# Kernel optimization log

Hardware: AMD Instinct MI355X
Metric: run time of the kernel (lower is better)

Reference implementation:

```python
import jax, jax.numpy as jnp
import numpy as np

NUM_HEADS = 12


def setup_inputs() -> dict:
    key = jax.random.key(0)
    k1, k2, k3, k4 = jax.random.split(key, 4)
    dim = 768
    B, N1, N2 = 8, 64, 4096  # N1 must equal head_dim = dim // num_heads
    x = jax.random.normal(k1, (B, N1, dim), dtype=jnp.float32)
    y = jax.random.normal(k2, (B, N2, dim), dtype=jnp.float32)
    # torch nn.Linear layout: [out_features, in_features]
    W_qkv = jax.random.normal(k3, (3 * dim, dim), dtype=jnp.float32) * 0.02
    W_proj = jax.random.normal(k4, (dim, dim), dtype=jnp.float32) * 0.02
    b_proj = jnp.zeros((dim,), dtype=jnp.float32)
    return {"x": x, "y": y, "W_qkv": W_qkv, "W_proj": W_proj, "b_proj": b_proj}


def _split_heads(t, H):
    # [B, N, C] -> [B, H, N, C//H]
    B, N, C = t.shape
    return t.reshape(B, N, H, C // H).transpose(0, 2, 1, 3)


def reference(x, y, W_qkv, W_proj, b_proj):
    H = NUM_HEADS
    B1, N1, C = x.shape
    B2, N2, _ = y.shape
    hd = C // H
    scale = hd ** -0.5

    # qkv projections (bias=False); take q from x, k/v from y
    qkv_x = x @ W_qkv.T                      # [B, N1, 3C]
    q = _split_heads(qkv_x[..., :C], H)      # [B, H, N1, hd]
    qkv_y = y @ W_qkv.T                      # [B, N2, 3C]
    k = _split_heads(qkv_y[..., C:2 * C], H)  # [B, H, N2, hd]
    v = _split_heads(qkv_y[..., 2 * C:], H)   # [B, H, N2, hd]

    attn = jnp.einsum('bhqd,bhkd->bhqk', q, k) * scale  # [B, H, N1, N2]
    attn = jax.nn.softmax(attn, axis=-1)
    attn_t = attn.transpose(0, 1, 3, 2)       # [B, H, N2, N1]; N1 == hd

    # non-standard elementwise combine with v (requires N1 == hd)
    out = attn_t * v                          # [B, H, N2, hd]
    out = out.transpose(0, 2, 1, 3).reshape(B2, N2, C)
    return out @ W_proj.T + b_proj
```

## Files before the change

### kernel.cpp

```cpp
#include <hip/hip_runtime.h>
#include <math.h>


typedef __attribute__((ext_vector_type(8))) short short8;
typedef __attribute__((ext_vector_type(4))) float f32x4;

__device__ __forceinline__ ushort f2bf(float x) {
  unsigned u = __float_as_uint(x);
  u += 0x7fffu + ((u >> 16) & 1u);
  return (ushort)(u >> 16);
}
__device__ __forceinline__ float bf2f(ushort h) {
  return __uint_as_float((unsigned)h << 16);
}

__device__ __forceinline__ void gl_lds16(const ushort* g, ushort* l) {
  __builtin_amdgcn_global_load_lds(
      (__attribute__((address_space(1))) void*)g,
      (__attribute__((address_space(3))) void*)l, 16, 0, 0);
}

__global__ __launch_bounds__(256) void cast_all(
    const float* __restrict__ x, ushort* __restrict__ xb,
    const float* __restrict__ w1, ushort* __restrict__ w1b,
    const float* __restrict__ w2, ushort* __restrict__ w2b,
    const float* __restrict__ y, ushort* __restrict__ yb) {
  long i = (long)(blockIdx.x * 256 + threadIdx.x) * 8;
  if (i >= 27918336L) return;
  const float* s; ushort* d; long off;
  if (i < 393216L)        { s = x;  d = xb;  off = i; }
  else if (i < 2162688L)  { s = w1; d = w1b; off = i - 393216L; }
  else if (i < 2752512L)  { s = w2; d = w2b; off = i - 2162688L; }
  else                    { s = y;  d = yb;  off = i - 2752512L; }
  float4 a = *(const float4*)(s + off);
  float4 b = *(const float4*)(s + off + 4);
  ushort o[8] = {f2bf(a.x), f2bf(a.y), f2bf(a.z), f2bf(a.w),
                 f2bf(b.x), f2bf(b.y), f2bf(b.z), f2bf(b.w)};
  *(uint4*)(d + off) = *(const uint4*)o;
}

template <typename CT>
__device__ __forceinline__ void gemm_body(
    const ushort* __restrict__ A, int lda,
    const ushort* __restrict__ B, int ldb,
    CT* __restrict__ C, int ldc, int K,
    const float* __restrict__ bias, int rt, int ct)
{
  __shared__ __align__(16) ushort As[3][4096];
  __shared__ __align__(16) ushort Bs[3][4096];
  const int tid = threadIdx.x;
  const int m0 = rt * 128, n0 = ct * 128;

  const int w = tid >> 6, lane = tid & 63;
  const int lm = lane & 15, quad = lane >> 4;
  const int wm = (w & 1) * 64, wn = (w >> 1) * 64;

  const int G0 = w * 64 + lane, G1 = G0 + 256;
  const int r0 = G0 >> 2, c0 = ((G0 & 3) - (r0 >> 1)) & 3;
  const int r1 = G1 >> 2, c1 = ((G1 & 3) - (r1 >> 1)) & 3;
  const ushort* Ag0 = A + (size_t)(m0 + r0) * lda + c0 * 8;
  const ushort* Ag1 = A + (size_t)(m0 + r1) * lda + c1 * 8;
  const ushort* Bg0 = B + (size_t)(n0 + r0) * ldb + c0 * 8;
  const ushort* Bg1 = B + (size_t)(n0 + r1) * ldb + c1 * 8;
  const int lds0 = w * 512, lds1 = w * 512 + 2048;

  f32x4 acc[4][4];
#pragma unroll
  for (int i = 0; i < 4; ++i)
#pragma unroll
    for (int j = 0; j < 4; ++j) acc[i][j] = (f32x4)(0.f);

  const int nk = K >> 5;
  gl_lds16(Ag0, &As[0][lds0]); gl_lds16(Ag1, &As[0][lds1]);
  gl_lds16(Bg0, &Bs[0][lds0]); gl_lds16(Bg1, &Bs[0][lds1]);
  gl_lds16(Ag0 + 32, &As[1][lds0]); gl_lds16(Ag1 + 32, &As[1][lds1]);
  gl_lds16(Bg0 + 32, &Bs[1][lds0]); gl_lds16(Bg1 + 32, &Bs[1][lds1]);
  asm volatile("s_waitcnt vmcnt(4)" ::: "memory");

  for (int kk = 0; kk < nk; ++kk) {
    __builtin_amdgcn_s_barrier();
    __builtin_amdgcn_sched_barrier(0);
    if (kk + 2 < nk) {
      const int k0 = (kk + 2) << 5;
      ushort* Ad = &As[(kk + 2) % 3][0];
      ushort* Bd = &Bs[(kk + 2) % 3][0];
      gl_lds16(Ag0 + k0, Ad + lds0); gl_lds16(Ag1 + k0, Ad + lds1);
      gl_lds16(Bg0 + k0, Bd + lds0); gl_lds16(Bg1 + k0, Bd + lds1);
    }
    const ushort* Ab = &As[kk % 3][0];
    const ushort* Bb = &Bs[kk % 3][0];
    short8 af[4], bf8[4];
#pragma unroll
    for (int i = 0; i < 4; ++i) {
      const int Ra = wm + i * 16 + lm;
      af[i] = *(const short8*)(const void*)(Ab + Ra * 32 + ((quad + (Ra >> 1)) & 3) * 8);
      const int Rb = wn + i * 16 + lm;
      bf8[i] = *(const short8*)(const void*)(Bb + Rb * 32 + ((quad + (Rb >> 1)) & 3) * 8);
    }
#pragma unroll
    for (int i = 0; i < 4; ++i)
#pragma unroll
      for (int j = 0; j < 4; ++j)
        acc[i][j] = __builtin_amdgcn_mfma_f32_16x16x32_bf16(af[i], bf8[j], acc[i][j], 0, 0, 0);
    if (kk < nk - 2)       asm volatile("s_waitcnt vmcnt(4)" ::: "memory");
    else if (kk == nk - 2) asm volatile("s_waitcnt vmcnt(0)" ::: "memory");
  }
  __syncthreads();

  if constexpr (sizeof(CT) == 2) {
    ushort* eb = ((ushort*)&Bs[0][0]) + w * 2048;
#pragma unroll
    for (int i = 0; i < 4; ++i) {
      ushort* ebc = eb + (i & 1) * 1024;
#pragma unroll
      for (int j = 0; j < 4; ++j)
#pragma unroll
        for (int r = 0; r < 4; ++r) {
          const int R = quad * 4 + r;
          const int gt = j * 2 + (lm >> 3);
          const int gs = (gt + R) & 7;
          ebc[R * 64 + gs * 8 + (lm & 7)] = f2bf(acc[i][j][r]);
        }
#pragma unroll
      for (int p = 0; p < 2; ++p) {
        const int R2 = (lane >> 3) + p * 8;
        const int g = lane & 7;
        const int gt2 = (g - R2) & 7;
        uint4 v = *(const uint4*)(const void*)(ebc + R2 * 64 + g * 8);
        *(uint4*)(C + (size_t)(m0 + wm + i * 16 + R2) * ldc + n0 + wn + gt2 * 8) = v;
      }
    }
  } else {
#pragma unroll
    for (int j = 0; j < 4; ++j) {
      const int col = n0 + wn + j * 16 + lm;
      const float bb = bias ? bias[col] : 0.f;
#pragma unroll
      for (int i = 0; i < 4; ++i) {
        const int row = m0 + wm + i * 16 + quad * 4;
#pragma unroll
        for (int r = 0; r < 4; ++r)
          C[(size_t)(row + r) * ldc + col] = (CT)(acc[i][j][r] + bb);
      }
    }
  }
}

__global__ __launch_bounds__(256) void qkv_gemm(
    const ushort* __restrict__ xbf, const ushort* __restrict__ ybf,
    const ushort* __restrict__ wqkv, ushort* __restrict__ qbf,
    ushort* __restrict__ kvbf)
{
  const int id = blockIdx.x;
  const ushort *A, *B; ushort* C; int ldc, rt, ct;
  if (id < 3072) {
    const int xcd = id & 7, local = id >> 3;
    const int per = 12 * 16;
    const int grp = local / per, s = local % per;
    rt = xcd * 32 + grp * 16 + (s & 15);
    ct = s >> 4;
    A = ybf; B = wqkv + (size_t)768 * 768; C = kvbf; ldc = 1536;
  } else {
    const int id2 = id - 3072;
    rt = id2 & 3; ct = id2 >> 2;
    A = xbf; B = wqkv; C = qbf; ldc = 768;
  }
  gemm_body<ushort>(A, 768, B, 768, C, ldc, 768, nullptr, rt, ct);
}

__global__ __launch_bounds__(256) void out_gemm(
    const ushort* __restrict__ Ebf, const ushort* __restrict__ wpbf,
    const float* __restrict__ bias, float* __restrict__ out)
{
  const int id = blockIdx.x;
  const int xcd = id & 7, local = id >> 3;
  const int per = 6 * 16;
  const int grp = local / per, s = local % per;
  const int rt = xcd * 32 + grp * 16 + (s & 15);
  const int ct = s >> 4;
  gemm_body<float>(Ebf, 768, wpbf, 768, out, 768, 768, bias, rt, ct);
}

__global__ __launch_bounds__(256) void attn_pass1(
    const ushort* __restrict__ Q,
    const ushort* __restrict__ KV,
    float* __restrict__ parts)
{
  const int chunk = blockIdx.x, h = blockIdx.y, b = blockIdx.z;
  const int tid = threadIdx.x;
  __shared__ __align__(16) ushort Qs[64 * 72];
  __shared__ __align__(16) ushort Ks[128 * 72];
  __shared__ float sm[4][64], ss[4][64];
#pragma unroll
  for (int p = 0; p < 2; ++p) {
    const int G = tid + 256 * p, row = G >> 3, g = G & 7;
    *(uint4*)(Qs + row * 72 + g * 8) =
        *(const uint4*)(Q + (size_t)(b * 64 + row) * 768 + h * 64 + g * 8);
  }
#pragma unroll
  for (int p = 0; p < 4; ++p) {
    const int G = tid + 256 * p, row = G >> 3, g = G & 7;
    *(uint4*)(Ks + row * 72 + g * 8) =
        *(const uint4*)(KV + (size_t)(b * 4096 + chunk * 128 + row) * 1536 + h * 64 + g * 8);
  }
  __syncthreads();

  const int w = tid >> 6, lane = tid & 63;
  const int lm = lane & 15, quad = lane >> 4;
  const int wn = w * 32;

  f32x4 acc[4][2];
#pragma unroll
  for (int i = 0; i < 4; ++i) { acc[i][0] = (f32x4)(0.f); acc[i][1] = (f32x4)(0.f); }
#pragma unroll
  for (int s = 0; s < 2; ++s) {
    short8 qf[4], kf[2];
#pragma unroll
    for (int i = 0; i < 4; ++i)
      qf[i] = *(const short8*)(const void*)(Qs + (i * 16 + lm) * 72 + s * 32 + quad * 8);
#pragma unroll
    for (int jn = 0; jn < 2; ++jn)
      kf[jn] = *(const short8*)(const void*)(Ks + (wn + jn * 16 + lm) * 72 + s * 32 + quad * 8);
#pragma unroll
    for (int i = 0; i < 4; ++i)
#pragma unroll
      for (int jn = 0; jn < 2; ++jn)
        acc[i][jn] = __builtin_amdgcn_mfma_f32_16x16x32_bf16(qf[i], kf[jn], acc[i][jn], 0, 0, 0);
  }

#pragma unroll
  for (int i = 0; i < 4; ++i)
#pragma unroll
    for (int r = 0; r < 4; ++r) {
      float v0 = acc[i][0][r] * 0.125f, v1 = acc[i][1][r] * 0.125f;
      float m = fmaxf(v0, v1);
      m = fmaxf(m, __shfl_xor(m, 1)); m = fmaxf(m, __shfl_xor(m, 2));
      m = fmaxf(m, __shfl_xor(m, 4)); m = fmaxf(m, __shfl_xor(m, 8));
      float e = __expf(v0 - m) + __expf(v1 - m);
      e += __shfl_xor(e, 1); e += __shfl_xor(e, 2);
      e += __shfl_xor(e, 4); e += __shfl_xor(e, 8);
      if (lm == 0) {
        const int j = i * 16 + quad * 4 + r;
        sm[w][j] = m; ss[w][j] = e;
      }
    }
  __syncthreads();
  if (tid < 64) {
    float g = fmaxf(fmaxf(sm[0][tid], sm[1][tid]), fmaxf(sm[2][tid], sm[3][tid]));
    float s = ss[0][tid] * __expf(sm[0][tid] - g) + ss[1][tid] * __expf(sm[1][tid] - g)
            + ss[2][tid] * __expf(sm[2][tid] - g) + ss[3][tid] * __expf(sm[3][tid] - g);
    const int bh = b * 12 + h;
    float* p = parts + ((size_t)(bh * 32 + chunk) * 64 + tid) * 2;
    p[0] = g; p[1] = s;
  }
}

__global__ __launch_bounds__(256) void attn_pass2(
    const ushort* __restrict__ Q, const ushort* __restrict__ KV,
    const float* __restrict__ parts, ushort* __restrict__ E)
{
  const int chunk = blockIdx.x, h = blockIdx.y, b = blockIdx.z;
  const int tid = threadIdx.x;
  __shared__ __align__(16) ushort Qs[64 * 72];
  __shared__ __align__(16) ushort Ks[128 * 72];
  __shared__ __align__(16) ushort Vs[128 * 72];
  __shared__ float st[64][2];
#pragma unroll
  for (int p = 0; p < 2; ++p) {
    const int G = tid + 256 * p, row = G >> 3, g = G & 7;
    *(uint4*)(Qs + row * 72 + g * 8) =
        *(const uint4*)(Q + (size_t)(b * 64 + row) * 768 + h * 64 + g * 8);
  }
#pragma unroll
  for (int p = 0; p < 4; ++p) {
    const int G = tid + 256 * p, row = G >> 3, g = G & 7;
    const size_t rbase = (size_t)(b * 4096 + chunk * 128 + row) * 1536 + h * 64 + g * 8;
    *(uint4*)(Ks + row * 72 + g * 8) = *(const uint4*)(KV + rbase);
    *(uint4*)(Vs + row * 72 + g * 8) = *(const uint4*)(KV + rbase + 768);
  }
  {
    const int bh = b * 12 + h;
    const int tq = tid >> 2, tc = tid & 3;
    float pm[8], ps[8];
    float gm = -1e30f;
#pragma unroll
    for (int c = 0; c < 8; ++c) {
      const float* p = parts + ((size_t)(bh * 32 + tc * 8 + c) * 64 + tq) * 2;
      pm[c] = p[0]; ps[c] = p[1];
      gm = fmaxf(gm, pm[c]);
    }
    gm = fmaxf(gm, __shfl_xor(gm, 1));
    gm = fmaxf(gm, __shfl_xor(gm, 2));
    float s = 0.f;
#pragma unroll
    for (int c = 0; c < 8; ++c) s += ps[c] * __expf(pm[c] - gm);
    s += __shfl_xor(s, 1);
    s += __shfl_xor(s, 2);
    if (tc == 0) { st[tq][0] = gm; st[tq][1] = 1.f / s; }
  }
  __syncthreads();

  const int w = tid >> 6, lane = tid & 63;
  const int lm = lane & 15, quad = lane >> 4;
  const int wn = w * 32;

  f32x4 acc[4][2];
#pragma unroll
  for (int i = 0; i < 4; ++i) { acc[i][0] = (f32x4)(0.f); acc[i][1] = (f32x4)(0.f); }
#pragma unroll
  for (int s = 0; s < 2; ++s) {
    short8 qf[4], kf[2];
#pragma unroll
    for (int i = 0; i < 4; ++i)
      qf[i] = *(const short8*)(const void*)(Qs + (i * 16 + lm) * 72 + s * 32 + quad * 8);
#pragma unroll
    for (int jn = 0; jn < 2; ++jn)
      kf[jn] = *(const short8*)(const void*)(Ks + (wn + jn * 16 + lm) * 72 + s * 32 + quad * 8);
#pragma unroll
    for (int i = 0; i < 4; ++i)
#pragma unroll
      for (int jn = 0; jn < 2; ++jn)
        acc[i][jn] = __builtin_amdgcn_mfma_f32_16x16x32_bf16(qf[i], kf[jn], acc[i][jn], 0, 0, 0);
  }

  ushort ev[4][2][4];
#pragma unroll
  for (int i = 0; i < 4; ++i)
#pragma unroll
    for (int jn = 0; jn < 2; ++jn)
#pragma unroll
      for (int r = 0; r < 4; ++r) {
        const float v = acc[i][jn][r] * 0.125f;
        const int j = i * 16 + quad * 4 + r;
        const float p = __expf(v - st[j][0]) * st[j][1];
        const int key = wn + jn * 16 + lm;
        ev[i][jn][r] = f2bf(p * bf2f(Vs[key * 72 + j]));
      }
  __syncthreads();
  ushort* Es = Ks;
#pragma unroll
  for (int i = 0; i < 4; ++i)
#pragma unroll
    for (int jn = 0; jn < 2; ++jn)
#pragma unroll
      for (int r = 0; r < 4; ++r)
        Es[(wn + jn * 16 + lm) * 72 + i * 16 + quad * 4 + r] = ev[i][jn][r];
  __syncthreads();
#pragma unroll
  for (int k = 0; k < 4; ++k) {
    const int row = tid >> 1, g = (tid & 1) * 4 + k;
    uint4 v = *(const uint4*)(const void*)(Es + row * 72 + g * 8);
    *(uint4*)(E + (size_t)(b * 4096 + chunk * 128 + row) * 768 + h * 64 + g * 8) = v;
  }
}

extern "C" void kernel_launch(void* const* d_in, const int* in_sizes, int n_in,
                              void* d_out, int out_size, void* d_ws, size_t ws_size,
                              hipStream_t stream) {
  const float* x     = (const float*)d_in[0];
  const float* y     = (const float*)d_in[1];
  const float* Wqkv  = (const float*)d_in[2];
  const float* Wproj = (const float*)d_in[3];
  const float* bproj = (const float*)d_in[4];
  float* out = (float*)d_out;

  char* wsb = (char*)d_ws;
  ushort* xbf    = (ushort*)(wsb + 0);
  ushort* qbf    = (ushort*)(wsb + 786432);
  ushort* wqkvbf = (ushort*)(wsb + 1572864);
  float*  parts  = (float*)(wsb + 1572864);
  ushort* wpbf   = (ushort*)(wsb + 5111808);
  ushort* ybf    = (ushort*)(wsb + 6291456);
  ushort* Ebf    = ybf;
  ushort* KVbf   = (ushort*)(wsb + 56623104);

  cast_all<<<13632, 256, 0, stream>>>(x, xbf, Wqkv, wqkvbf, Wproj, wpbf, y, ybf);

  qkv_gemm<<<3096, 256, 0, stream>>>(xbf, ybf, wqkvbf, qbf, KVbf);

  attn_pass1<<<dim3(32, 12, 8), 256, 0, stream>>>(qbf, KVbf, parts);
  attn_pass2<<<dim3(32, 12, 8), 256, 0, stream>>>(qbf, KVbf, parts, Ebf);

  out_gemm<<<1536, 256, 0, stream>>>(Ebf, wpbf, bproj, out);
}
```

Measured before the change: 405.4 us.

## Enlarge GEMM tiles to 256x128 with double buffering and remap grids

The shared GEMM body moves from 128x128 tiles with a three-stage LDS ring to 256x128 tiles with two-stage buffering. Each wave now computes a 128x64 sub-tile of 8x4 MFMA fragments, which raises B-operand reuse and halves the number of blocks for the QKV and output projections. The explicit vmcnt waits are replaced by plain __syncthreads, and launch bounds request two blocks per CU. The risks are a shallower prefetch pipeline, higher register use from the doubled accumulators, and fewer blocks to spread across the CUs.

```diff
diff --git a/kernel.cpp b/kernel.cpp
--- a/kernel.cpp
+++ b/kernel.cpp
@@ -46,71 +46,78 @@
     CT* __restrict__ C, int ldc, int K,
     const float* __restrict__ bias, int rt, int ct)
 {
-  __shared__ __align__(16) ushort As[3][4096];
-  __shared__ __align__(16) ushort Bs[3][4096];
+  __shared__ __align__(16) ushort As[2][8192];
+  __shared__ __align__(16) ushort Bs[2][4096];
   const int tid = threadIdx.x;
-  const int m0 = rt * 128, n0 = ct * 128;
+  const int m0 = rt * 256, n0 = ct * 128;
 
   const int w = tid >> 6, lane = tid & 63;
   const int lm = lane & 15, quad = lane >> 4;
-  const int wm = (w & 1) * 64, wn = (w >> 1) * 64;
-
-  const int G0 = w * 64 + lane, G1 = G0 + 256;
-  const int r0 = G0 >> 2, c0 = ((G0 & 3) - (r0 >> 1)) & 3;
-  const int r1 = G1 >> 2, c1 = ((G1 & 3) - (r1 >> 1)) & 3;
-  const ushort* Ag0 = A + (size_t)(m0 + r0) * lda + c0 * 8;
-  const ushort* Ag1 = A + (size_t)(m0 + r1) * lda + c1 * 8;
-  const ushort* Bg0 = B + (size_t)(n0 + r0) * ldb + c0 * 8;
-  const ushort* Bg1 = B + (size_t)(n0 + r1) * ldb + c1 * 8;
-  const int lds0 = w * 512, lds1 = w * 512 + 2048;
-
-  f32x4 acc[4][4];
-#pragma unroll
-  for (int i = 0; i < 4; ++i)
+  const int WR = (w >> 1) * 128, WC = (w & 1) * 64;
+
+  const ushort* Ag[4];
+#pragma unroll
+  for (int q = 0; q < 4; ++q) {
+    const int G = q * 256 + w * 64 + lane;
+    const int row = G >> 2, g = ((G & 3) - (row >> 1)) & 3;
+    Ag[q] = A + (size_t)(m0 + row) * lda + g * 8;
+  }
+  const ushort* Bg[2];
+#pragma unroll
+  for (int q = 0; q < 2; ++q) {
+    const int G = q * 256 + w * 64 + lane;
+    const int row = G >> 2, g = ((G & 3) - (row >> 1)) & 3;
+    Bg[q] = B + (size_t)(n0 + row) * ldb + g * 8;
+  }
+
+  f32x4 acc[8][4];
+#pragma unroll
+  for (int i = 0; i < 8; ++i)
 #pragma unroll
     for (int j = 0; j < 4; ++j) acc[i][j] = (f32x4)(0.f);
 
   const int nk = K >> 5;
-  gl_lds16(Ag0, &As[0][lds0]); gl_lds16(Ag1, &As[0][lds1]);
-  gl_lds16(Bg0, &Bs[0][lds0]); gl_lds16(Bg1, &Bs[0][lds1]);
-  gl_lds16(Ag0 + 32, &As[1][lds0]); gl_lds16(Ag1 + 32, &As[1][lds1]);
-  gl_lds16(Bg0 + 32, &Bs[1][lds0]); gl_lds16(Bg1 + 32, &Bs[1][lds1]);
-  asm volatile("s_waitcnt vmcnt(4)" ::: "memory");
-
+#pragma unroll
+  for (int q = 0; q < 4; ++q) gl_lds16(Ag[q], &As[0][q * 2048 + w * 512]);
+#pragma unroll
+  for (int q = 0; q < 2; ++q) gl_lds16(Bg[q], &Bs[0][q * 2048 + w * 512]);
+
+  int cur = 0;
   for (int kk = 0; kk < nk; ++kk) {
-    __builtin_amdgcn_s_barrier();
-    __builtin_amdgcn_sched_barrier(0);
-    if (kk + 2 < nk) {
-      const int k0 = (kk + 2) << 5;
-      ushort* Ad = &As[(kk + 2) % 3][0];
-      ushort* Bd = &Bs[(kk + 2) % 3][0];
-      gl_lds16(Ag0 + k0, Ad + lds0); gl_lds16(Ag1 + k0, Ad + lds1);
-      gl_lds16(Bg0 + k0, Bd + lds0); gl_lds16(Bg1 + k0, Bd + lds1);
-    }
-    const ushort* Ab = &As[kk % 3][0];
-    const ushort* Bb = &Bs[kk % 3][0];
-    short8 af[4], bf8[4];
-#pragma unroll
-    for (int i = 0; i < 4; ++i) {
-      const int Ra = wm + i * 16 + lm;
+    __syncthreads();
+    if (kk + 1 < nk) {
+      const int k0 = (kk + 1) << 5;
+#pragma unroll
+      for (int q = 0; q < 4; ++q) gl_lds16(Ag[q] + k0, &As[cur ^ 1][q * 2048 + w * 512]);
+#pragma unroll
+      for (int q = 0; q < 2; ++q) gl_lds16(Bg[q] + k0, &Bs[cur ^ 1][q * 2048 + w * 512]);
+    }
+    const ushort* Ab = &As[cur][0];
+    const ushort* Bb = &Bs[cur][0];
+    short8 af[8], bf8[4];
+#pragma unroll
+    for (int i = 0; i < 8; ++i) {
+      const int Ra = WR + i * 16 + lm;
       af[i] = *(const short8*)(const void*)(Ab + Ra * 32 + ((quad + (Ra >> 1)) & 3) * 8);
-      const int Rb = wn + i * 16 + lm;
-      bf8[i] = *(const short8*)(const void*)(Bb + Rb * 32 + ((quad + (Rb >> 1)) & 3) * 8);
-    }
-#pragma unroll
-    for (int i = 0; i < 4; ++i)
+    }
+#pragma unroll
+    for (int j = 0; j < 4; ++j) {
+      const int Rb = WC + j * 16 + lm;
+      bf8[j] = *(const short8*)(const void*)(Bb + Rb * 32 + ((quad + (Rb >> 1)) & 3) * 8);
+    }
+#pragma unroll
+    for (int i = 0; i < 8; ++i)
 #pragma unroll
       for (int j = 0; j < 4; ++j)
         acc[i][j] = __builtin_amdgcn_mfma_f32_16x16x32_bf16(af[i], bf8[j], acc[i][j], 0, 0, 0);
-    if (kk < nk - 2)       asm volatile("s_waitcnt vmcnt(4)" ::: "memory");
-    else if (kk == nk - 2) asm volatile("s_waitcnt vmcnt(0)" ::: "memory");
+    cur ^= 1;
   }
   __syncthreads();
 
   if constexpr (sizeof(CT) == 2) {
-    ushort* eb = ((ushort*)&Bs[0][0]) + w * 2048;
-#pragma unroll
-    for (int i = 0; i < 4; ++i) {
+    ushort* eb = ((ushort*)&As[0][0]) + w * 2048;
+#pragma unroll
+    for (int i = 0; i < 8; ++i) {
       ushort* ebc = eb + (i & 1) * 1024;
 #pragma unroll
       for (int j = 0; j < 4; ++j)
@@ -127,17 +134,17 @@
         const int g = lane & 7;
         const int gt2 = (g - R2) & 7;
         uint4 v = *(const uint4*)(const void*)(ebc + R2 * 64 + g * 8);
-        *(uint4*)(C + (size_t)(m0 + wm + i * 16 + R2) * ldc + n0 + wn + gt2 * 8) = v;
+        *(uint4*)(C + (size_t)(m0 + WR + i * 16 + R2) * ldc + n0 + WC + gt2 * 8) = v;
       }
     }
   } else {
 #pragma unroll
     for (int j = 0; j < 4; ++j) {
-      const int col = n0 + wn + j * 16 + lm;
+      const int col = n0 + WC + j * 16 + lm;
       const float bb = bias ? bias[col] : 0.f;
 #pragma unroll
-      for (int i = 0; i < 4; ++i) {
-        const int row = m0 + wm + i * 16 + quad * 4;
+      for (int i = 0; i < 8; ++i) {
+        const int row = m0 + WR + i * 16 + quad * 4;
 #pragma unroll
         for (int r = 0; r < 4; ++r)
           C[(size_t)(row + r) * ldc + col] = (CT)(acc[i][j][r] + bb);
@@ -146,38 +153,32 @@
   }
 }
 
-__global__ __launch_bounds__(256) void qkv_gemm(
+__global__ __launch_bounds__(256, 2) void qkv_gemm(
     const ushort* __restrict__ xbf, const ushort* __restrict__ ybf,
     const ushort* __restrict__ wqkv, ushort* __restrict__ qbf,
     ushort* __restrict__ kvbf)
 {
   const int id = blockIdx.x;
-  const ushort *A, *B; ushort* C; int ldc, rt, ct;
-  if (id < 3072) {
+  if (id < 1536) {
     const int xcd = id & 7, local = id >> 3;
-    const int per = 12 * 16;
-    const int grp = local / per, s = local % per;
-    rt = xcd * 32 + grp * 16 + (s & 15);
-    ct = s >> 4;
-    A = ybf; B = wqkv + (size_t)768 * 768; C = kvbf; ldc = 1536;
+    const int rt = xcd * 16 + (local & 15);
+    const int ct = local >> 4;
+    gemm_body<ushort>(ybf, 768, wqkv + (size_t)768 * 768, 768, kvbf, 1536, 768,
+                      nullptr, rt, ct);
   } else {
-    const int id2 = id - 3072;
-    rt = id2 & 3; ct = id2 >> 2;
-    A = xbf; B = wqkv; C = qbf; ldc = 768;
-  }
-  gemm_body<ushort>(A, 768, B, 768, C, ldc, 768, nullptr, rt, ct);
-}
-
-__global__ __launch_bounds__(256) void out_gemm(
+    const int q = id - 1536;
+    gemm_body<ushort>(xbf, 768, wqkv, 768, qbf, 768, 768, nullptr, q & 1, q >> 1);
+  }
+}
+
+__global__ __launch_bounds__(256, 2) void out_gemm(
     const ushort* __restrict__ Ebf, const ushort* __restrict__ wpbf,
     const float* __restrict__ bias, float* __restrict__ out)
 {
   const int id = blockIdx.x;
   const int xcd = id & 7, local = id >> 3;
-  const int per = 6 * 16;
-  const int grp = local / per, s = local % per;
-  const int rt = xcd * 32 + grp * 16 + (s & 15);
-  const int ct = s >> 4;
+  const int rt = xcd * 16 + (local & 15);
+  const int ct = local >> 4;
   gemm_body<float>(Ebf, 768, wpbf, 768, out, 768, 768, bias, rt, ct);
 }
 
@@ -376,10 +377,10 @@
 
   cast_all<<<13632, 256, 0, stream>>>(x, xbf, Wqkv, wqkvbf, Wproj, wpbf, y, ybf);
 
-  qkv_gemm<<<3096, 256, 0, stream>>>(xbf, ybf, wqkvbf, qbf, KVbf);
+  qkv_gemm<<<1548, 256, 0, stream>>>(xbf, ybf, wqkvbf, qbf, KVbf);
 
   attn_pass1<<<dim3(32, 12, 8), 256, 0, stream>>>(qbf, KVbf, parts);
   attn_pass2<<<dim3(32, 12, 8), 256, 0, stream>>>(qbf, KVbf, parts, Ebf);
 
-  out_gemm<<<1536, 256, 0, stream>>>(Ebf, wpbf, bproj, out);
-}
+  out_gemm<<<768, 256, 0, stream>>>(Ebf, wpbf, bproj, out);
+}
```

New measurement: 427.3 us. 5.4% more time.
